# Optimization experiments

Hardware: AMD Instinct MI355X
Metric: run time of the kernel (lower is better)

## Reference

```python
import jax, jax.numpy as jnp
import numpy as np

D_MODEL = 1024
NUM_HEADS = 16
D_K = D_MODEL // NUM_HEADS


def setup_inputs() -> dict:
    key = jax.random.key(0)
    kq, kwq, kwk, kwv, kwo = jax.random.split(key, 5)
    B, S = 4, 2048
    Q = jax.random.normal(kq, (B, S, D_MODEL), dtype=jnp.float32)
    # causal mask, broadcastable to (B, H, Sq, Sk); mask==0 -> -1e9
    mask = jnp.tril(jnp.ones((S, S), dtype=jnp.int32))[None, None]
    scale = 1.0 / np.sqrt(D_MODEL)
    W_q = jax.random.normal(kwq, (D_MODEL, D_MODEL), dtype=jnp.float32) * scale
    W_k = jax.random.normal(kwk, (D_MODEL, D_MODEL), dtype=jnp.float32) * scale
    W_v = jax.random.normal(kwv, (D_MODEL, D_MODEL), dtype=jnp.float32) * scale
    W_o = jax.random.normal(kwo, (D_MODEL, D_MODEL), dtype=jnp.float32) * scale
    return {"Q": Q, "W_q": W_q, "W_k": W_k, "W_v": W_v, "W_o": W_o, "mask": mask}


def _split_heads(x):
    B, S, _ = x.shape
    return x.reshape(B, S, NUM_HEADS, D_K).transpose(0, 2, 1, 3)  # (B,H,S,Dk)


def reference(Q, W_q, W_k, W_v, W_o, mask):
    # self-attention path: K = V = Q (inputs), dropout=0 (identity)
    q = _split_heads(Q @ W_q.T)
    k = _split_heads(Q @ W_k.T)
    v = _split_heads(Q @ W_v.T)
    scores = jnp.einsum('bhqd,bhkd->bhqk', q, k) / jnp.sqrt(jnp.float32(D_K))
    scores = jnp.where(mask == 0, jnp.float32(-1e9), scores)
    attn = jax.nn.softmax(scores, axis=-1)
    out = jnp.einsum('bhqk,bhkd->bhqd', attn, v)  # (B,H,S,Dk)
    B, H, S, Dk = out.shape
    out = out.transpose(0, 2, 1, 3).reshape(B, S, H * Dk)
    return out @ W_o.T
```

## Files before the change

kernel.cpp:

```cpp
#include <hip/hip_runtime.h>
#include <hip/hip_bf16.h>
#include <stdint.h>

typedef __attribute__((ext_vector_type(8))) short s8v;
typedef __attribute__((ext_vector_type(4))) float f4v;
typedef __attribute__((ext_vector_type(4))) unsigned short us4v;
typedef __attribute__((ext_vector_type(2))) unsigned int u32x2;

#define MFMA16(a,b,c) __builtin_amdgcn_mfma_f32_16x16x32_bf16((a),(b),(c),0,0,0)

#if __has_builtin(__builtin_amdgcn_exp2f)
#define EXP2(x) __builtin_amdgcn_exp2f(x)
#else
#define EXP2(x) exp2f(x)
#endif

__device__ __forceinline__ unsigned short bfu(float x){
  __hip_bfloat16 h = __float2bfloat16(x);
  return __builtin_bit_cast(unsigned short, h);
}

__device__ __forceinline__ void gload_lds16(const void* g, void* l){
  __builtin_amdgcn_global_load_lds((const __attribute__((address_space(1))) unsigned int*)g,
                                   (__attribute__((address_space(3))) unsigned int*)l,
                                   16, 0, 0);
}

__global__ __launch_bounds__(256) void k_convert(
    const float* __restrict__ Q,  const float* __restrict__ W0,
    const float* __restrict__ W1, const float* __restrict__ W2,
    const float* __restrict__ W3, unsigned short* __restrict__ dst){
  int t = blockIdx.x*256 + threadIdx.x;
  int e = t*4;
  const float* src; int off;
  if (e < 8388608)       { src = Q;  off = e; }
  else if (e < 9437184)  { src = W0; off = e - 8388608; }
  else if (e < 10485760) { src = W1; off = e - 9437184; }
  else if (e < 11534336) { src = W2; off = e - 10485760; }
  else                   { src = W3; off = e - 11534336; }
  float4 v = *(const float4*)(src + off);
  us4v o = { bfu(v.x), bfu(v.y), bfu(v.z), bfu(v.w) };
  *(us4v*)(dst + e) = o;
}

__device__ __forceinline__ void gemm_core(const unsigned short* __restrict__ A,
                                          const unsigned short* __restrict__ B,
                                          int m0, int n0, unsigned short* lds,
                                          f4v acc[4][4]){
  const int tid = threadIdx.x, wave = tid>>6, lane = tid&63, lq = lane&15, g = lane>>4;
  const int wr = wave>>1, wc = wave&1;
  char* ldsA = (char*)lds;
  char* ldsB = (char*)lds + 8192;
  for (int kt = 0; kt < 1024; kt += 32){
    __syncthreads();
    #pragma unroll
    for (int i = 0; i < 2; ++i){
      int L = (i*256 + tid)*16;
      int row = L>>6, ssw = (L>>4)&3;
      int gcol = kt + ((ssw ^ ((row>>1)&3))<<3);
      gload_lds16(A + (m0 + row)*1024 + gcol, ldsA + i*4096 + wave*1024);
      gload_lds16(B + (n0 + row)*1024 + gcol, ldsB + i*4096 + wave*1024);
    }
    __syncthreads();
    s8v af[4], bf[4];
    #pragma unroll
    for (int mi = 0; mi < 4; ++mi){
      int row = wr*64 + mi*16 + lq;
      af[mi] = *(const s8v*)(ldsA + row*64 + ((g ^ ((row>>1)&3))<<4));
    }
    #pragma unroll
    for (int ni = 0; ni < 4; ++ni){
      int row = wc*64 + ni*16 + lq;
      bf[ni] = *(const s8v*)(ldsB + row*64 + ((g ^ ((row>>1)&3))<<4));
    }
    #pragma unroll
    for (int mi = 0; mi < 4; ++mi)
      #pragma unroll
      for (int ni = 0; ni < 4; ++ni)
        acc[mi][ni] = MFMA16(af[mi], bf[ni], acc[mi][ni]);
  }
}

__global__ __launch_bounds__(256) void k_qkv(
    const unsigned short* __restrict__ xb,
    const unsigned short* __restrict__ wq, const unsigned short* __restrict__ wk,
    const unsigned short* __restrict__ wv,
    unsigned short* __restrict__ qb, unsigned short* __restrict__ kb,
    unsigned short* __restrict__ vtb){
  __shared__ unsigned short lds[8192];
  const int m0 = blockIdx.x*128;
  const int by = blockIdx.y, wsel = by>>3, n0 = (by&7)*128;
  const unsigned short* B = (wsel==0)? wq : ((wsel==1)? wk : wv);
  f4v acc[4][4] = {};
  gemm_core(xb, B, m0, n0, lds, acc);
  const int tid = threadIdx.x, wave = tid>>6, lane = tid&63, lq = lane&15, g = lane>>4;
  const int wr = wave>>1, wc = wave&1;
  if (wsel == 2){
    #pragma unroll
    for (int mi = 0; mi < 4; ++mi){
      int mbase = m0 + wr*64 + mi*16 + g*4;
      int b = mbase>>11, s = mbase&2047;
      #pragma unroll
      for (int ni = 0; ni < 4; ++ni){
        int n = n0 + wc*64 + ni*16 + lq;
        int h = n>>6, d = n&63;
        f4v a = acc[mi][ni];
        us4v p = { bfu(a[0]), bfu(a[1]), bfu(a[2]), bfu(a[3]) };
        *(us4v*)(vtb + ((b*16 + h)*64 + d)*2048 + s) = p;
      }
    }
  } else {
    unsigned short* dst = wsel ? kb : qb;
    char* tb = (char*)lds + wave*4096;
    const int hh = (n0 + wc*64)>>6;
    __syncthreads();
    #pragma unroll
    for (int h2 = 0; h2 < 2; ++h2){
      #pragma unroll
      for (int mi2 = 0; mi2 < 2; ++mi2){
        int mi = h2*2 + mi2;
        #pragma unroll
        for (int ni = 0; ni < 4; ++ni){
          f4v a = acc[mi][ni];
          #pragma unroll
          for (int i = 0; i < 4; ++i){
            int s_loc = mi2*16 + g*4 + i;
            int d_loc = ni*16 + lq;
            int addr = s_loc*128 + (((d_loc>>2) ^ (s_loc&15))<<3) + ((d_loc&3)<<1);
            *(unsigned short*)(tb + addr) = bfu(a[i]);
          }
        }
      }
      #pragma unroll
      for (int j = 0; j < 8; ++j){
        int s_loc = j*4 + g;
        int m = m0 + wr*64 + h2*32 + s_loc;
        int b = m>>11, s = m&2047;
        int d_loc = lq*4;
        int addr = s_loc*128 + ((lq ^ (s_loc&15))<<3);
        u32x2 v = *(const u32x2*)(tb + addr);
        *(u32x2*)(dst + ((b*16 + hh)*2048 + s)*64 + d_loc) = v;
      }
      if (h2 == 0) __syncthreads();
    }
  }
}

#define CSCL 0.18033688011112042f
__global__ __launch_bounds__(256, 2) void k_attn(
    const unsigned short* __restrict__ qbuf, const unsigned short* __restrict__ kbuf,
    const unsigned short* __restrict__ vtbuf, unsigned short* __restrict__ ao){
  __shared__ unsigned short lds[32768];
  char* ldsK = (char*)lds;
  char* ldsV = (char*)lds + 16384;
  const int tid = threadIdx.x, wave = tid>>6, lane = tid&63, lq = lane&15, g = lane>>4;
  char* ldsP = (char*)lds + 32768 + wave*8192;
  const int bh = blockIdx.x;
  const int qt = 15 - blockIdx.y;
  const int qbase = qt*128;
  const unsigned short* qh = qbuf  + bh*131072;
  const unsigned short* kh = kbuf  + bh*131072;
  const unsigned short* vh = vtbuf + bh*131072;

  s8v qf_[2][2];
  #pragma unroll
  for (int qf = 0; qf < 2; ++qf)
    #pragma unroll
    for (int ks = 0; ks < 2; ++ks){
      int row = qbase + wave*32 + qf*16 + lq;
      qf_[qf][ks] = *(const s8v*)(qh + row*64 + ks*32 + g*8);
    }

  f4v ot[4][2] = {};
  float lrow[2] = {0.f, 0.f};

  for (int kt = 0; kt <= qt; ++kt){
    int kbase = kt*128;
    __syncthreads();
    #pragma unroll
    for (int i = 0; i < 4; ++i){
      int L = (i*256 + tid)*16;
      { int row = L>>7, ssw = (L>>4)&7;
        gload_lds16(kh + (kbase + row)*64 + ((ssw ^ (row&7))<<3),
                    ldsK + i*4096 + wave*1024); }
      { int d = L>>8, ssw = (L>>4)&15;
        gload_lds16(vh + d*2048 + kbase + ((ssw ^ (d&7))<<3),
                    ldsV + i*4096 + wave*1024); }
    }
    __syncthreads();

    f4v sf[8][2];
    #pragma unroll
    for (int kf = 0; kf < 8; ++kf){
      s8v ka[2];
      #pragma unroll
      for (int ks = 0; ks < 2; ++ks){
        int row = kf*16 + lq;
        ka[ks] = *(const s8v*)(ldsK + row*128 + (((4*ks + g) ^ (row&7))<<4));
      }
      #pragma unroll
      for (int qf = 0; qf < 2; ++qf){
        f4v s = {};
        s = MFMA16(ka[0], qf_[qf][0], s);
        s = MFMA16(ka[1], qf_[qf][1], s);
        sf[kf][qf] = s;
      }
    }

    #pragma unroll
    for (int qf = 0; qf < 2; ++qf){
      int qg = qbase + wave*32 + qf*16 + lq;
      if (kt == qt){
        #pragma unroll
        for (int kf = 0; kf < 8; ++kf)
          #pragma unroll
          for (int i = 0; i < 4; ++i){
            int kgl = kbase + kf*16 + g*4 + i;
            if (kgl > qg) sf[kf][qf][i] = -1e30f;
          }
      }
      float ps = 0.f;
      int q_l = qf*16 + lq;
      #pragma unroll
      for (int kf = 0; kf < 8; ++kf){
        f4v s = sf[kf][qf];
        float p0 = EXP2(s[0]*CSCL);
        float p1 = EXP2(s[1]*CSCL);
        float p2 = EXP2(s[2]*CSCL);
        float p3 = EXP2(s[3]*CSCL);
        ps += (p0+p1) + (p2+p3);
        unsigned int lo = (unsigned int)bfu(p0) | ((unsigned int)bfu(p1)<<16);
        unsigned int hi = (unsigned int)bfu(p2) | ((unsigned int)bfu(p3)<<16);
        int k0 = kf*16 + g*4;
        int byte = q_l*256 + (((k0>>3) ^ (q_l&7))<<4) + ((k0&7)<<1);
        u32x2 pk = { lo, hi };
        *(u32x2*)(ldsP + byte) = pk;
      }
      lrow[qf] += ps;
    }

    #pragma unroll
    for (int ks = 0; ks < 4; ++ks){
      s8v va[4], pb[2];
      #pragma unroll
      for (int df = 0; df < 4; ++df){
        int row = df*16 + lq;
        va[df] = *(const s8v*)(ldsV + row*256 + (((4*ks + g) ^ (row&7))<<4));
      }
      #pragma unroll
      for (int qf = 0; qf < 2; ++qf){
        int q_l = qf*16 + lq;
        pb[qf] = *(const s8v*)(ldsP + q_l*256 + (((4*ks + g) ^ (q_l&7))<<4));
      }
      #pragma unroll
      for (int df = 0; df < 4; ++df)
        #pragma unroll
        for (int qf = 0; qf < 2; ++qf)
          ot[df][qf] = MFMA16(va[df], pb[qf], ot[df][qf]);
    }
  }

  const int b = bh>>4, h = bh&15;
  #pragma unroll
  for (int qf = 0; qf < 2; ++qf){
    float l = lrow[qf];
    l += __shfl_xor(l, 16);
    l += __shfl_xor(l, 32);
    float rin = 1.f / l;
    int qg = qbase + wave*32 + qf*16 + lq;
    int rowoff = (b*2048 + qg)*1024 + h*64;
    #pragma unroll
    for (int df = 0; df < 4; ++df){
      f4v o = ot[df][qf];
      us4v p = { bfu(o[0]*rin), bfu(o[1]*rin), bfu(o[2]*rin), bfu(o[3]*rin) };
      *(us4v*)(ao + rowoff + df*16 + g*4) = p;
    }
  }
}

__global__ __launch_bounds__(256) void k_out(
    const unsigned short* __restrict__ aob, const unsigned short* __restrict__ wo,
    float* __restrict__ out){
  __shared__ unsigned short lds[8192];
  const int m0 = blockIdx.x*128, n0 = blockIdx.y*128;
  f4v acc[4][4] = {};
  gemm_core(aob, wo, m0, n0, lds, acc);
  const int tid = threadIdx.x, wave = tid>>6, lane = tid&63, lq = lane&15, g = lane>>4;
  const int wr = wave>>1, wc = wave&1;
  #pragma unroll
  for (int mi = 0; mi < 4; ++mi){
    int mbase = m0 + wr*64 + mi*16 + g*4;
    #pragma unroll
    for (int ni = 0; ni < 4; ++ni){
      int n = n0 + wc*64 + ni*16 + lq;
      f4v a = acc[mi][ni];
      #pragma unroll
      for (int i = 0; i < 4; ++i)
        out[(mbase + i)*1024 + n] = a[i];
    }
  }
}

extern "C" void kernel_launch(void* const* d_in, const int* in_sizes, int n_in,
                              void* d_out, int out_size, void* d_ws, size_t ws_size,
                              hipStream_t stream){
  const float* Q  = (const float*)d_in[0];
  const float* Wq = (const float*)d_in[1];
  const float* Wk = (const float*)d_in[2];
  const float* Wv = (const float*)d_in[3];
  const float* Wo = (const float*)d_in[4];

  unsigned short* ws   = (unsigned short*)d_ws;
  unsigned short* xb   = ws;
  unsigned short* wqb  = ws + 8388608;
  unsigned short* wkb  = ws + 9437184;
  unsigned short* wvb  = ws + 10485760;
  unsigned short* wob  = ws + 11534336;
  unsigned short* qbuf = ws + 12582912;
  unsigned short* kbuf = ws + 20971520;
  unsigned short* vtb  = ws + 29360128;
  unsigned short* aob  = ws;

  k_convert<<<12288, 256, 0, stream>>>(Q, Wq, Wk, Wv, Wo, ws);
  k_qkv<<<dim3(64, 24), 256, 0, stream>>>(xb, wqb, wkb, wvb, qbuf, kbuf, vtb);
  k_attn<<<dim3(64, 16), 256, 0, stream>>>(qbuf, kbuf, vtb, aob);
  k_out<<<dim3(64, 8), 256, 0, stream>>>(aob, wob, (float*)d_out);
}
```

Measured before the change: 265.3 us.

## Double-buffer LDS tiles in GEMMs and attention, split softmax/PV into halves

Both GEMM cores and the attention kernel now prefetch the next K/V (or A/B) tile into a second LDS buffer while computing on the current one, cutting one barrier per iteration. The attention P buffer is halved and the softmax/PV work is interleaved in two halves, with MFMA sections raised in wave priority. This aims to hide global-to-LDS latency behind compute, at the cost of doubled LDS footprint, which may limit occupancy.

New measurement: 254.4 us. -4.1%, faster.

```diff
diff --git a/kernel.cpp b/kernel.cpp
--- a/kernel.cpp
+++ b/kernel.cpp
@@ -43,41 +43,51 @@
   *(us4v*)(dst + e) = o;
 }
 
+__device__ __forceinline__ void gemm_stage(const unsigned short* __restrict__ A,
+                                           const unsigned short* __restrict__ B,
+                                           int m0, int n0, int t, char* lds,
+                                           int tid, int wave){
+  char* dA = lds + (t&1)*16384;
+  char* dB = dA + 8192;
+  #pragma unroll
+  for (int i = 0; i < 2; ++i){
+    int si = i*256 + tid;
+    int row = si>>2, s = si&3;
+    int gcol = t*32 + ((s ^ ((row>>1)&3))<<3);
+    gload_lds16(A + (m0 + row)*1024 + gcol, dA + i*4096 + wave*1024);
+    gload_lds16(B + (n0 + row)*1024 + gcol, dB + i*4096 + wave*1024);
+  }
+}
+
 __device__ __forceinline__ void gemm_core(const unsigned short* __restrict__ A,
                                           const unsigned short* __restrict__ B,
-                                          int m0, int n0, unsigned short* lds,
+                                          int m0, int n0, char* lds,
                                           f4v acc[4][4]){
   const int tid = threadIdx.x, wave = tid>>6, lane = tid&63, lq = lane&15, g = lane>>4;
   const int wr = wave>>1, wc = wave&1;
-  char* ldsA = (char*)lds;
-  char* ldsB = (char*)lds + 8192;
-  for (int kt = 0; kt < 1024; kt += 32){
-    __syncthreads();
-    #pragma unroll
-    for (int i = 0; i < 2; ++i){
-      int L = (i*256 + tid)*16;
-      int row = L>>6, ssw = (L>>4)&3;
-      int gcol = kt + ((ssw ^ ((row>>1)&3))<<3);
-      gload_lds16(A + (m0 + row)*1024 + gcol, ldsA + i*4096 + wave*1024);
-      gload_lds16(B + (n0 + row)*1024 + gcol, ldsB + i*4096 + wave*1024);
-    }
-    __syncthreads();
+  gemm_stage(A, B, m0, n0, 0, lds, tid, wave);
+  __syncthreads();
+  for (int t = 0; t < 32; ++t){
+    if (t < 31) gemm_stage(A, B, m0, n0, t+1, lds, tid, wave);
+    char* cA = lds + (t&1)*16384;
+    char* cB = cA + 8192;
     s8v af[4], bf[4];
     #pragma unroll
     for (int mi = 0; mi < 4; ++mi){
       int row = wr*64 + mi*16 + lq;
-      af[mi] = *(const s8v*)(ldsA + row*64 + ((g ^ ((row>>1)&3))<<4));
+      af[mi] = *(const s8v*)(cA + row*64 + ((g ^ ((row>>1)&3))<<4));
     }
     #pragma unroll
     for (int ni = 0; ni < 4; ++ni){
       int row = wc*64 + ni*16 + lq;
-      bf[ni] = *(const s8v*)(ldsB + row*64 + ((g ^ ((row>>1)&3))<<4));
+      bf[ni] = *(const s8v*)(cB + row*64 + ((g ^ ((row>>1)&3))<<4));
     }
     #pragma unroll
     for (int mi = 0; mi < 4; ++mi)
       #pragma unroll
       for (int ni = 0; ni < 4; ++ni)
         acc[mi][ni] = MFMA16(af[mi], bf[ni], acc[mi][ni]);
+    __syncthreads();
   }
 }
 
@@ -87,12 +97,12 @@
     const unsigned short* __restrict__ wv,
     unsigned short* __restrict__ qb, unsigned short* __restrict__ kb,
     unsigned short* __restrict__ vtb){
-  __shared__ unsigned short lds[8192];
+  __shared__ unsigned short lds[16384];
   const int m0 = blockIdx.x*128;
   const int by = blockIdx.y, wsel = by>>3, n0 = (by&7)*128;
   const unsigned short* B = (wsel==0)? wq : ((wsel==1)? wk : wv);
   f4v acc[4][4] = {};
-  gemm_core(xb, B, m0, n0, lds, acc);
+  gemm_core(xb, B, m0, n0, (char*)lds, acc);
   const int tid = threadIdx.x, wave = tid>>6, lane = tid&63, lq = lane&15, g = lane>>4;
   const int wr = wave>>1, wc = wave&1;
   if (wsel == 2){
@@ -150,11 +160,11 @@
 __global__ __launch_bounds__(256, 2) void k_attn(
     const unsigned short* __restrict__ qbuf, const unsigned short* __restrict__ kbuf,
     const unsigned short* __restrict__ vtbuf, unsigned short* __restrict__ ao){
-  __shared__ unsigned short lds[32768];
+  __shared__ unsigned short lds[40960];
   char* ldsK = (char*)lds;
-  char* ldsV = (char*)lds + 16384;
+  char* ldsV = (char*)lds + 32768;
   const int tid = threadIdx.x, wave = tid>>6, lane = tid&63, lq = lane&15, g = lane>>4;
-  char* ldsP = (char*)lds + 32768 + wave*8192;
+  char* ldsP = (char*)lds + 65536 + wave*4096;
   const int bh = blockIdx.x;
   const int qt = 15 - blockIdx.y;
   const int qbase = qt*128;
@@ -174,20 +184,40 @@
   f4v ot[4][2] = {};
   float lrow[2] = {0.f, 0.f};
 
+  {
+    int kb = 0;
+    #pragma unroll
+    for (int i = 0; i < 4; ++i){
+      int si = i*256 + tid;
+      { int row = si>>3, s = si&7;
+        gload_lds16(kh + (kb + row)*64 + ((s ^ (row&7))<<3),
+                    ldsK + i*4096 + wave*1024); }
+      { int d = si>>4, s = si&15;
+        gload_lds16(vh + d*2048 + kb + ((s ^ (d&7))<<3),
+                    ldsV + i*4096 + wave*1024); }
+    }
+  }
+  __syncthreads();
+
   for (int kt = 0; kt <= qt; ++kt){
     int kbase = kt*128;
-    __syncthreads();
-    #pragma unroll
-    for (int i = 0; i < 4; ++i){
-      int L = (i*256 + tid)*16;
-      { int row = L>>7, ssw = (L>>4)&7;
-        gload_lds16(kh + (kbase + row)*64 + ((ssw ^ (row&7))<<3),
-                    ldsK + i*4096 + wave*1024); }
-      { int d = L>>8, ssw = (L>>4)&15;
-        gload_lds16(vh + d*2048 + kbase + ((ssw ^ (d&7))<<3),
-                    ldsV + i*4096 + wave*1024); }
-    }
-    __syncthreads();
+    if (kt < qt){
+      int kb = kbase + 128;
+      char* dK = ldsK + ((kt+1)&1)*16384;
+      char* dV = ldsV + ((kt+1)&1)*16384;
+      #pragma unroll
+      for (int i = 0; i < 4; ++i){
+        int si = i*256 + tid;
+        { int row = si>>3, s = si&7;
+          gload_lds16(kh + (kb + row)*64 + ((s ^ (row&7))<<3),
+                      dK + i*4096 + wave*1024); }
+        { int d = si>>4, s = si&15;
+          gload_lds16(vh + d*2048 + kb + ((s ^ (d&7))<<3),
+                      dV + i*4096 + wave*1024); }
+      }
+    }
+    char* cK = ldsK + (kt&1)*16384;
+    char* cV = ldsV + (kt&1)*16384;
 
     f4v sf[8][2];
     #pragma unroll
@@ -196,7 +226,7 @@
       #pragma unroll
       for (int ks = 0; ks < 2; ++ks){
         int row = kf*16 + lq;
-        ka[ks] = *(const s8v*)(ldsK + row*128 + (((4*ks + g) ^ (row&7))<<4));
+        ka[ks] = *(const s8v*)(cK + row*128 + (((4*ks + g) ^ (row&7))<<4));
       }
       #pragma unroll
       for (int qf = 0; qf < 2; ++qf){
@@ -208,56 +238,60 @@
     }
 
     #pragma unroll
-    for (int qf = 0; qf < 2; ++qf){
-      int qg = qbase + wave*32 + qf*16 + lq;
-      if (kt == qt){
-        #pragma unroll
-        for (int kf = 0; kf < 8; ++kf)
+    for (int hf = 0; hf < 2; ++hf){
+      #pragma unroll
+      for (int qf = 0; qf < 2; ++qf){
+        int qg = qbase + wave*32 + qf*16 + lq;
+        int q_l = qf*16 + lq;
+        float ps = 0.f;
+        #pragma unroll
+        for (int kf2 = 0; kf2 < 4; ++kf2){
+          int kf = hf*4 + kf2;
+          f4v s = sf[kf][qf];
+          if (kt == qt){
+            #pragma unroll
+            for (int i = 0; i < 4; ++i){
+              int kgl = kbase + kf*16 + g*4 + i;
+              if (kgl > qg) s[i] = -1e30f;
+            }
+          }
+          float p0 = EXP2(s[0]*CSCL);
+          float p1 = EXP2(s[1]*CSCL);
+          float p2 = EXP2(s[2]*CSCL);
+          float p3 = EXP2(s[3]*CSCL);
+          ps += (p0+p1) + (p2+p3);
+          unsigned int lo = (unsigned int)bfu(p0) | ((unsigned int)bfu(p1)<<16);
+          unsigned int hi = (unsigned int)bfu(p2) | ((unsigned int)bfu(p3)<<16);
+          int byte = q_l*128 + (((kf2*2 + (g>>1)) ^ (q_l&7))<<4) + ((g&1)<<3);
+          u32x2 pk = { lo, hi };
+          *(u32x2*)(ldsP + byte) = pk;
+        }
+        lrow[qf] += ps;
+      }
+      __builtin_amdgcn_s_setprio(1);
+      #pragma unroll
+      for (int ks2 = 0; ks2 < 2; ++ks2){
+        int ks = hf*2 + ks2;
+        s8v va[4], pb[2];
+        #pragma unroll
+        for (int df = 0; df < 4; ++df){
+          int row = df*16 + lq;
+          va[df] = *(const s8v*)(cV + row*256 + (((4*ks + g) ^ (row&7))<<4));
+        }
+        #pragma unroll
+        for (int qf = 0; qf < 2; ++qf){
+          int q_l = qf*16 + lq;
+          pb[qf] = *(const s8v*)(ldsP + q_l*128 + (((ks2*4 + g) ^ (q_l&7))<<4));
+        }
+        #pragma unroll
+        for (int df = 0; df < 4; ++df)
           #pragma unroll
-          for (int i = 0; i < 4; ++i){
-            int kgl = kbase + kf*16 + g*4 + i;
-            if (kgl > qg) sf[kf][qf][i] = -1e30f;
-          }
-      }
-      float ps = 0.f;
-      int q_l = qf*16 + lq;
-      #pragma unroll
-      for (int kf = 0; kf < 8; ++kf){
-        f4v s = sf[kf][qf];
-        float p0 = EXP2(s[0]*CSCL);
-        float p1 = EXP2(s[1]*CSCL);
-        float p2 = EXP2(s[2]*CSCL);
-        float p3 = EXP2(s[3]*CSCL);
-        ps += (p0+p1) + (p2+p3);
-        unsigned int lo = (unsigned int)bfu(p0) | ((unsigned int)bfu(p1)<<16);
-        unsigned int hi = (unsigned int)bfu(p2) | ((unsigned int)bfu(p3)<<16);
-        int k0 = kf*16 + g*4;
-        int byte = q_l*256 + (((k0>>3) ^ (q_l&7))<<4) + ((k0&7)<<1);
-        u32x2 pk = { lo, hi };
-        *(u32x2*)(ldsP + byte) = pk;
-      }
-      lrow[qf] += ps;
-    }
-
-    #pragma unroll
-    for (int ks = 0; ks < 4; ++ks){
-      s8v va[4], pb[2];
-      #pragma unroll
-      for (int df = 0; df < 4; ++df){
-        int row = df*16 + lq;
-        va[df] = *(const s8v*)(ldsV + row*256 + (((4*ks + g) ^ (row&7))<<4));
-      }
-      #pragma unroll
-      for (int qf = 0; qf < 2; ++qf){
-        int q_l = qf*16 + lq;
-        pb[qf] = *(const s8v*)(ldsP + q_l*256 + (((4*ks + g) ^ (q_l&7))<<4));
-      }
-      #pragma unroll
-      for (int df = 0; df < 4; ++df)
-        #pragma unroll
-        for (int qf = 0; qf < 2; ++qf)
-          ot[df][qf] = MFMA16(va[df], pb[qf], ot[df][qf]);
-    }
+          for (int qf = 0; qf < 2; ++qf)
+            ot[df][qf] = MFMA16(va[df], pb[qf], ot[df][qf]);
+      }
+      __builtin_amdgcn_s_setprio(0);
+    }
+    __syncthreads();
   }
 
   const int b = bh>>4, h = bh&15;
@@ -281,10 +315,10 @@
 __global__ __launch_bounds__(256) void k_out(
     const unsigned short* __restrict__ aob, const unsigned short* __restrict__ wo,
     float* __restrict__ out){
-  __shared__ unsigned short lds[8192];
+  __shared__ unsigned short lds[16384];
   const int m0 = blockIdx.x*128, n0 = blockIdx.y*128;
   f4v acc[4][4] = {};
-  gemm_core(aob, wo, m0, n0, lds, acc);
+  gemm_core(aob, wo, m0, n0, (char*)lds, acc);
   const int tid = threadIdx.x, wave = tid>>6, lane = tid&63, lq = lane&15, g = lane>>4;
   const int wr = wave>>1, wc = wave&1;
   #pragma unroll
```
